# Kernel optimization log

Measured on AMD Instinct MI355X. Metric: run time of the kernel, lower is better.

## Reference

```python
import jax, jax.numpy as jnp
import numpy as np

EPS = 1e-5
GROUPS = 32

def group_norm(x, w, b):
    B, C, H, W = x.shape
    g = GROUPS
    xr = x.reshape(B, g, C // g, H * W)
    mean = xr.mean(axis=(2, 3), keepdims=True)
    var = xr.var(axis=(2, 3), keepdims=True)
    h = ((xr - mean) / jnp.sqrt(var + EPS)).reshape(B, C, H, W)
    return h * w[None, :, None, None] + b[None, :, None, None]

def setup_inputs() -> dict:
    key = jax.random.key(0)
    ks = jax.random.split(key, 7)
    B, C, H, W = 8, 256, 64, 64
    d = C // 8  # 32
    x = jax.random.normal(ks[0], (B, C, H, W), dtype=jnp.float32)
    norm_w = 1.0 + 0.1 * jax.random.normal(ks[1], (C,), dtype=jnp.float32)
    norm_b = 0.1 * jax.random.normal(ks[2], (C,), dtype=jnp.float32)
    s = 1.0 / np.sqrt(C)
    Wq = jax.random.normal(ks[3], (d, C), dtype=jnp.float32) * s
    Wk = jax.random.normal(ks[4], (d, C), dtype=jnp.float32) * s
    Wv = jax.random.normal(ks[5], (C, C), dtype=jnp.float32) * s
    Wproj = jax.random.normal(ks[6], (C, C), dtype=jnp.float32) * s
    gamma = jnp.full((1,), 0.5, dtype=jnp.float32)  # torch init is 0; nonzero so attention path contributes
    return {"x": x, "norm_w": norm_w, "norm_b": norm_b, "Wq": Wq, "Wk": Wk,
            "Wv": Wv, "Wproj": Wproj, "gamma": gamma}

def reference(x, norm_w, norm_b, Wq, Wk, Wv, Wproj, gamma):
    B, C, H, W = x.shape
    N = H * W
    h = group_norm(x, norm_w, norm_b)           # (B,C,H,W)
    hf = h.reshape(B, C, N)                      # flatten spatial
    d = Wq.shape[0]
    q = jnp.einsum('dc,bcn->bnd', Wq, hf)        # (B,N,d)
    k = jnp.einsum('dc,bcn->bdn', Wk, hf)        # (B,d,N)
    v = jnp.einsum('oc,bcn->bno', Wv, hf)        # (B,N,C)
    scale = d ** (-0.5)
    attn = jax.nn.softmax(jnp.einsum('bnd,bdm->bnm', q, k) * scale, axis=-1)  # (B,N,N)
    out = jnp.einsum('bnm,bmo->bno', attn, v)    # (B,N,C)
    out = out.transpose(0, 2, 1).reshape(B, C, H, W)
    proj = jnp.einsum('oc,bchw->bohw', Wproj, out)
    return x + gamma[0] * proj
```

## Files before the change

### kernel.cpp

```cpp
#include <hip/hip_runtime.h>
#include <cstdint>


typedef __bf16 bf16x8 __attribute__((ext_vector_type(8)));
typedef float f32x4 __attribute__((ext_vector_type(4)));
typedef float f32x16 __attribute__((ext_vector_type(16)));
typedef unsigned int u32x4 __attribute__((ext_vector_type(4)));
typedef unsigned short u16x4 __attribute__((ext_vector_type(4)));
typedef unsigned short u16x8 __attribute__((ext_vector_type(8)));

#define DEVI __device__ __forceinline__

DEVI unsigned short f2bf(float f) {
    __bf16 h = (__bf16)f;
    return __builtin_bit_cast(unsigned short, h);
}
DEVI float bf2f(unsigned short u) {
    unsigned int x = ((unsigned int)u) << 16;
    return __builtin_bit_cast(float, x);
}

DEVI f32x4 mfma16(bf16x8 a, bf16x8 b, f32x4 c) {
    return __builtin_amdgcn_mfma_f32_16x16x32_bf16(a, b, c, 0, 0, 0);
}
DEVI f32x16 mfma32(bf16x8 a, bf16x8 b, f32x16 c) {
    return __builtin_amdgcn_mfma_f32_32x32x16_bf16(a, b, c, 0, 0, 0);
}

DEVI void glds16(const unsigned short* g, unsigned short* l) {
    const __attribute__((address_space(1))) unsigned int* gp =
        reinterpret_cast<const __attribute__((address_space(1))) unsigned int*>(
            reinterpret_cast<uintptr_t>(g));
    __attribute__((address_space(3))) unsigned int* lp =
        reinterpret_cast<__attribute__((address_space(3))) unsigned int*>(
            reinterpret_cast<uintptr_t>(l));
    __builtin_amdgcn_global_load_lds(gp, lp, 16, 0, 0);
}

#define QSCALE 0.2550663133f
#define MFIX   12.0f

__global__ __launch_bounds__(256) void k_pack(
        const float* __restrict__ wq, const float* __restrict__ wk,
        const float* __restrict__ wv, const float* __restrict__ wp,
        unsigned short* __restrict__ bqk, unsigned short* __restrict__ bv,
        unsigned short* __restrict__ bp) {
    int i = blockIdx.x * 256 + threadIdx.x;
    if (i < 8192)       bqk[i] = f2bf(wq[i] * QSCALE);
    else if (i < 16384) bqk[i] = f2bf(wk[i - 8192]);
    bv[i] = f2bf(wv[i]);
    bp[i] = f2bf(wp[i]);
}

__global__ __launch_bounds__(1024) void k_gnorm(
        const float* __restrict__ x, const float* __restrict__ gw,
        const float* __restrict__ gb, unsigned short* __restrict__ ht) {
    int bg = blockIdx.x;
    int b = bg >> 5, g = bg & 31;
    const float* xb = x + ((size_t)(b * 256 + g * 8)) * 4096;
    int t = threadIdx.x;
    float s1 = 0.f, s2 = 0.f;
    const f32x4* xv4 = (const f32x4*)xb;
    for (int i = t; i < 8192; i += 1024) {
        f32x4 v = xv4[i];
        #pragma unroll
        for (int j = 0; j < 4; j++) { s1 += v[j]; s2 += v[j] * v[j]; }
    }
    #pragma unroll
    for (int off = 1; off < 64; off <<= 1) {
        s1 += __shfl_xor(s1, off);
        s2 += __shfl_xor(s2, off);
    }
    __shared__ float red[34];
    int wv_ = t >> 6;
    if ((t & 63) == 0) { red[wv_ * 2] = s1; red[wv_ * 2 + 1] = s2; }
    __syncthreads();
    if (t == 0) {
        float a = 0.f, q = 0.f;
        #pragma unroll
        for (int i = 0; i < 16; i++) { a += red[i * 2]; q += red[i * 2 + 1]; }
        float mean = a * (1.f / 32768.f);
        float var = q * (1.f / 32768.f) - mean * mean;
        red[32] = mean; red[33] = rsqrtf(var + 1e-5f);
    }
    __syncthreads();
    float mean = red[32], rstd = red[33];
    float wv8[8], bv8[8];
    #pragma unroll
    for (int c = 0; c < 8; c++) { wv8[c] = gw[g * 8 + c] * rstd; bv8[c] = gb[g * 8 + c] - mean * rstd * gw[g * 8 + c]; }
    int n0 = t * 4;
    f32x4 cv[8];
    #pragma unroll
    for (int c = 0; c < 8; c++) cv[c] = *(const f32x4*)(xb + c * 4096 + n0);
    #pragma unroll
    for (int j = 0; j < 4; j++) {
        u16x8 pk;
        #pragma unroll
        for (int c = 0; c < 8; c++) pk[c] = f2bf(cv[c][j] * wv8[c] + bv8[c]);
        *(u16x8*)(&ht[((size_t)(b * 4096 + n0 + j)) * 256 + g * 8]) = pk;
    }
}

template <int EPI>
__global__ __launch_bounds__(256) void k_gemm(
        const unsigned short* __restrict__ A, const unsigned short* __restrict__ Bw,
        void* __restrict__ outp, const float* __restrict__ xres,
        const float* __restrict__ gamma, int ldout) {
    __shared__ unsigned short lA[128 * 72];
    __shared__ unsigned short lB[64 * 72];
    int t = threadIdx.x;
    int m0 = blockIdx.x * 128, n0 = blockIdx.y * 64;
    int w = t >> 6, lane = t & 63, l15 = lane & 15, quad = lane >> 4;
    f32x4 z4 = {0.f, 0.f, 0.f, 0.f};
    f32x4 acc[2][4];
    #pragma unroll
    for (int i = 0; i < 2; i++)
        #pragma unroll
        for (int j = 0; j < 4; j++) acc[i][j] = z4;

    for (int kb = 0; kb < 4; kb++) {
        #pragma unroll
        for (int i = 0; i < 4; i++) {
            int ch = i * 256 + t;
            int row = ch >> 3, col = (ch & 7) * 8;
            u32x4 v = *(const u32x4*)(A + (size_t)(m0 + row) * 256 + kb * 64 + col);
            *(u32x4*)(&lA[row * 72 + col]) = v;
        }
        #pragma unroll
        for (int i = 0; i < 2; i++) {
            int ch = i * 256 + t;
            int row = ch >> 3, col = (ch & 7) * 8;
            u32x4 v = *(const u32x4*)(Bw + (size_t)(n0 + row) * 256 + kb * 64 + col);
            *(u32x4*)(&lB[row * 72 + col]) = v;
        }
        __syncthreads();
        #pragma unroll
        for (int ks = 0; ks < 2; ks++) {
            bf16x8 af[2], bfr[4];
            #pragma unroll
            for (int fr = 0; fr < 2; fr++)
                af[fr] = *(const bf16x8*)(&lA[(w * 32 + fr * 16 + l15) * 72 + ks * 32 + quad * 8]);
            #pragma unroll
            for (int fn = 0; fn < 4; fn++)
                bfr[fn] = *(const bf16x8*)(&lB[(fn * 16 + l15) * 72 + ks * 32 + quad * 8]);
            #pragma unroll
            for (int fr = 0; fr < 2; fr++)
                #pragma unroll
                for (int fn = 0; fn < 4; fn++)
                    acc[fr][fn] = mfma16(af[fr], bfr[fn], acc[fr][fn]);
        }
        __syncthreads();
    }

    if (EPI == 0) {
        unsigned short* out = (unsigned short*)outp;
        #pragma unroll
        for (int fr = 0; fr < 2; fr++)
            #pragma unroll
            for (int fn = 0; fn < 4; fn++)
                #pragma unroll
                for (int r = 0; r < 4; r++) {
                    int m = m0 + w * 32 + fr * 16 + quad * 4 + r;
                    int n = n0 + fn * 16 + l15;
                    out[(size_t)m * ldout + n] = f2bf(acc[fr][fn][r]);
                }
    } else if (EPI == 1) {
        unsigned short* out = (unsigned short*)outp;
        int b = m0 >> 12, nb = (m0 & 4095) + w * 32;
        int swq = ((quad & 1) << 1) | (quad >> 1);
        #pragma unroll
        for (int fr = 0; fr < 2; fr++)
            #pragma unroll
            for (int fn = 0; fn < 4; fn++) {
                int o = n0 + fn * 16 + l15;
                int n = nb + fr * 16 + swq * 4;
                u16x4 pk;
                #pragma unroll
                for (int r = 0; r < 4; r++) pk[r] = f2bf(acc[fr][fn][r]);
                *(u16x4*)(&out[(((size_t)(b * 256 + o)) << 12) + n]) = pk;
            }
    } else {
        float* out = (float*)outp;
        float gm = gamma[0];
        int b = m0 >> 12, nb = (m0 & 4095) + w * 32;
        #pragma unroll
        for (int fr = 0; fr < 2; fr++)
            #pragma unroll
            for (int fn = 0; fn < 4; fn++) {
                int o = n0 + fn * 16 + l15;
                int n = nb + fr * 16 + quad * 4;
                size_t base = (((size_t)(b * 256 + o)) << 12) + n;
                f32x4 xv = *(const f32x4*)(xres + base);
                f32x4 ov;
                #pragma unroll
                for (int r = 0; r < 4; r++) ov[r] = xv[r] + gm * acc[fr][fn][r];
                *(f32x4*)(out + base) = ov;
            }
    }
}

__global__ __launch_bounds__(256, 2) void k_flash(
        const unsigned short* __restrict__ QK, const unsigned short* __restrict__ Vt,
        unsigned short* __restrict__ Oa) {
    __shared__ __align__(16) char smem[40960];
    unsigned short* lK = (unsigned short*)smem;
    unsigned short* lV = (unsigned short*)(smem + 4096);
    int id = blockIdx.x;
    int b = id & 7, qt = id >> 3;
    int t = threadIdx.x, w = t >> 6, ln = t & 63;
    int l31 = ln & 31, h = ln >> 5;
    int qh = w >> 1, kh = w & 1;
    int q0 = qt * 64;

    const unsigned short* qrow = QK + ((size_t)(b * 4096 + q0 + qh * 32 + l31)) * 64;
    bf16x8 qb0 = *(const bf16x8*)(qrow + h * 8);
    bf16x8 qb1 = *(const bf16x8*)(qrow + 16 + h * 8);

    int cgK = (ln & 3) ^ ((ln >> 2) & 3) ^ ((ln >> 4) & 3);
    const unsigned short* gK = QK + ((size_t)(b * 4096 + w * 16 + (ln >> 2))) * 64 + 32 + cgK * 8;
    unsigned short* sK = lK + w * 512;
    int vc8 = (ln & 7) ^ ((ln >> 3) & 7);
    const unsigned short* gV = Vt + (((size_t)(b * 256 + w * 64 + (ln >> 3))) << 12) + vc8 * 8;
    unsigned short* sV = lV + w * 4096;

    u16x8 onesu = {0x3F80, 0x3F80, 0x3F80, 0x3F80, 0x3F80, 0x3F80, 0x3F80, 0x3F80};
    bf16x8 ones = __builtin_bit_cast(bf16x8, onesu);
    f32x16 z16;
    #pragma unroll
    for (int i = 0; i < 16; i++) z16[i] = 0.f;
    f32x16 minit;
    #pragma unroll
    for (int i = 0; i < 16; i++) minit[i] = -MFIX;
    f32x16 Oacc[8];
    #pragma unroll
    for (int i = 0; i < 8; i++) Oacc[i] = z16;
    f32x16 lacc = z16;

    int gl = (ln & 3) ^ ((ln >> 2) & 3);
    const unsigned short* kf0p = lK + (kh * 32 + l31) * 32 + ((0 + h) ^ gl) * 8;
    const unsigned short* kf1p = lK + (kh * 32 + l31) * 32 + ((2 + h) ^ gl) * 8;

    for (int kt = 0; kt < 64; kt++) {
        glds16(gK + (size_t)kt * 4096, sK);
        #pragma unroll
        for (int j = 0; j < 8; j++)
            glds16(gV + ((size_t)j * 8 << 12) + kt * 64, sV + j * 512);
        __syncthreads();

        bf16x8 kf0 = *(const bf16x8*)kf0p;
        bf16x8 kf1 = *(const bf16x8*)kf1p;
        f32x16 St = mfma32(kf0, qb0, minit);
        St = mfma32(kf1, qb1, St);

        u16x8 p0u, p1u;
        #pragma unroll
        for (int j = 0; j < 8; j++) {
            p0u[j] = f2bf(__builtin_amdgcn_exp2f(St[j]));
            p1u[j] = f2bf(__builtin_amdgcn_exp2f(St[8 + j]));
        }
        bf16x8 pa0 = __builtin_bit_cast(bf16x8, p0u);
        bf16x8 pa1 = __builtin_bit_cast(bf16x8, p1u);

        lacc = mfma32(pa0, ones, lacc);
        lacc = mfma32(pa1, ones, lacc);

        #pragma unroll
        for (int s2 = 0; s2 < 2; s2++) {
            bf16x8 pa = s2 ? pa1 : pa0;
            int slot = ((kh * 4 + s2 * 2 + h) ^ (ln & 7)) * 8;
            #pragma unroll
            for (int nt = 0; nt < 8; nt++) {
                bf16x8 vf = *(const bf16x8*)(lV + (nt * 32 + l31) * 64 + slot);
                Oacc[nt] = mfma32(pa, vf, Oacc[nt]);
            }
        }
        __syncthreads();
    }

    if (kh == 1) {
        #pragma unroll
        for (int nt = 0; nt < 8; nt++)
            #pragma unroll
            for (int rg = 0; rg < 2; rg++) {
                u16x8 pk;
                #pragma unroll
                for (int j = 0; j < 8; j++) pk[j] = f2bf(Oacc[nt][rg * 8 + j]);
                *(u16x8*)(smem + qh * 16384 + nt * 2048 + rg * 1024 + ln * 16) = pk;
            }
        #pragma unroll
        for (int rg = 0; rg < 4; rg++) {
            f32x4 lv;
            #pragma unroll
            for (int j = 0; j < 4; j++) lv[j] = lacc[rg * 4 + j];
            *(f32x4*)(smem + 32768 + qh * 4096 + rg * 1024 + ln * 16) = lv;
        }
    }
    __syncthreads();
    if (kh == 0) {
        float rl[16];
        #pragma unroll
        for (int rg = 0; rg < 4; rg++) {
            f32x4 lv = *(const f32x4*)(smem + 32768 + qh * 4096 + rg * 1024 + ln * 16);
            #pragma unroll
            for (int j = 0; j < 4; j++) rl[rg * 4 + j] = 1.f / (lacc[rg * 4 + j] + lv[j]);
        }
        size_t rb = (size_t)(b * 4096 + q0 + qh * 32);
        #pragma unroll
        for (int nt = 0; nt < 8; nt++)
            #pragma unroll
            for (int rg = 0; rg < 2; rg++) {
                u16x8 pk = *(const u16x8*)(smem + qh * 16384 + nt * 2048 + rg * 1024 + ln * 16);
                #pragma unroll
                for (int j = 0; j < 8; j++) {
                    int r = rg * 8 + j;
                    float val = (Oacc[nt][r] + bf2f(pk[j])) * rl[r];
                    int row = (r & 3) + 8 * (r >> 2) + 4 * h;
                    Oa[(rb + row) * 256 + nt * 32 + l31] = f2bf(val);
                }
            }
    }
}

extern "C" void kernel_launch(void* const* d_in, const int* in_sizes, int n_in,
                              void* d_out, int out_size, void* d_ws, size_t ws_size,
                              hipStream_t stream) {
    const float* x  = (const float*)d_in[0];
    const float* nw = (const float*)d_in[1];
    const float* nb = (const float*)d_in[2];
    const float* wq = (const float*)d_in[3];
    const float* wk = (const float*)d_in[4];
    const float* wv = (const float*)d_in[5];
    const float* wp = (const float*)d_in[6];
    const float* gm = (const float*)d_in[7];

    char* p = (char*)d_ws;
    unsigned short* ht  = (unsigned short*)p; p += (size_t)32768 * 256 * 2;
    unsigned short* qk  = (unsigned short*)p; p += (size_t)32768 * 64 * 2;
    unsigned short* vt  = (unsigned short*)p; p += (size_t)8 * 256 * 4096 * 2;
    unsigned short* oa  = (unsigned short*)p; p += (size_t)32768 * 256 * 2;
    unsigned short* bqk = (unsigned short*)p; p += 64 * 256 * 2;
    unsigned short* bv  = (unsigned short*)p; p += 256 * 256 * 2;
    unsigned short* bp  = (unsigned short*)p; p += 256 * 256 * 2;

    k_pack<<<dim3(256), dim3(256), 0, stream>>>(wq, wk, wv, wp, bqk, bv, bp);
    k_gnorm<<<dim3(256), dim3(1024), 0, stream>>>(x, nw, nb, ht);
    k_gemm<0><<<dim3(256, 1), dim3(256), 0, stream>>>(ht, bqk, (void*)qk, nullptr, nullptr, 64);
    k_gemm<1><<<dim3(256, 4), dim3(256), 0, stream>>>(ht, bv, (void*)vt, nullptr, nullptr, 0);
    k_flash<<<dim3(512), dim3(256), 0, stream>>>(qk, vt, oa);
    k_gemm<2><<<dim3(256, 4), dim3(256), 0, stream>>>(oa, bp, d_out, x, gm, 0);
}
```

Measured before the change: 236.1 us.

## Double-buffer K/V LDS tiles in flash kernel to overlap loads with MFMA

Doubles the flash-attention kernel's shared memory to hold two K/V tile buffers. The loop is unrolled by two so the async global-to-LDS copy of the next tile is issued before computing on the current one. Each step syncs with a raw barrier plus a vmcnt(0) wait instead of two __syncthreads. The goal is to hide global load latency behind the QK/PV MFMA work. The cost is 72KB of LDS per block, which limits occupancy to two blocks per CU.

```diff
diff --git a/kernel.cpp b/kernel.cpp
--- a/kernel.cpp
+++ b/kernel.cpp
@@ -35,6 +35,15 @@
         reinterpret_cast<__attribute__((address_space(3))) unsigned int*>(
             reinterpret_cast<uintptr_t>(l));
     __builtin_amdgcn_global_load_lds(gp, lp, 16, 0, 0);
+}
+
+DEVI void barrier_raw() {
+    asm volatile("" ::: "memory");
+    __builtin_amdgcn_s_barrier();
+    asm volatile("" ::: "memory");
+}
+DEVI void wait_vm0() {
+    __builtin_amdgcn_s_waitcnt(0x3F70);
 }
 
 #define QSCALE 0.2550663133f
@@ -202,9 +211,7 @@
 __global__ __launch_bounds__(256, 2) void k_flash(
         const unsigned short* __restrict__ QK, const unsigned short* __restrict__ Vt,
         unsigned short* __restrict__ Oa) {
-    __shared__ __align__(16) char smem[40960];
-    unsigned short* lK = (unsigned short*)smem;
-    unsigned short* lV = (unsigned short*)(smem + 4096);
+    __shared__ __align__(16) char smem[73728];
     int id = blockIdx.x;
     int b = id & 7, qt = id >> 3;
     int t = threadIdx.x, w = t >> 6, ln = t & 63;
@@ -218,10 +225,17 @@
 
     int cgK = (ln & 3) ^ ((ln >> 2) & 3) ^ ((ln >> 4) & 3);
     const unsigned short* gK = QK + ((size_t)(b * 4096 + w * 16 + (ln >> 2))) * 64 + 32 + cgK * 8;
-    unsigned short* sK = lK + w * 512;
     int vc8 = (ln & 7) ^ ((ln >> 3) & 7);
     const unsigned short* gV = Vt + (((size_t)(b * 256 + w * 64 + (ln >> 3))) << 12) + vc8 * 8;
-    unsigned short* sV = lV + w * 4096;
+
+    unsigned short* lK0 = (unsigned short*)smem;
+    unsigned short* lV0 = (unsigned short*)(smem + 4096);
+    unsigned short* lK1 = (unsigned short*)(smem + 36864);
+    unsigned short* lV1 = (unsigned short*)(smem + 36864 + 4096);
+    unsigned short* sK0 = lK0 + w * 512;
+    unsigned short* sV0 = lV0 + w * 4096;
+    unsigned short* sK1 = lK1 + w * 512;
+    unsigned short* sV1 = lV1 + w * 4096;
 
     u16x8 onesu = {0x3F80, 0x3F80, 0x3F80, 0x3F80, 0x3F80, 0x3F80, 0x3F80, 0x3F80};
     bf16x8 ones = __builtin_bit_cast(bf16x8, onesu);
@@ -236,22 +250,27 @@
     for (int i = 0; i < 8; i++) Oacc[i] = z16;
     f32x16 lacc = z16;
 
-    int gl = (ln & 3) ^ ((ln >> 2) & 3);
-    const unsigned short* kf0p = lK + (kh * 32 + l31) * 32 + ((0 + h) ^ gl) * 8;
-    const unsigned short* kf1p = lK + (kh * 32 + l31) * 32 + ((2 + h) ^ gl) * 8;
-
-    for (int kt = 0; kt < 64; kt++) {
-        glds16(gK + (size_t)kt * 4096, sK);
+    int gl = (l31 & 3) ^ ((l31 >> 2) & 3);
+    const unsigned short* kf0p0 = lK0 + (kh * 32 + l31) * 32 + ((0 + h) ^ gl) * 8;
+    const unsigned short* kf1p0 = lK0 + (kh * 32 + l31) * 32 + ((2 + h) ^ gl) * 8;
+    const unsigned short* kf0p1 = lK1 + (kh * 32 + l31) * 32 + ((0 + h) ^ gl) * 8;
+    const unsigned short* kf1p1 = lK1 + (kh * 32 + l31) * 32 + ((2 + h) ^ gl) * 8;
+    int slotA = ((kh * 4 + 0 * 2 + h) ^ (ln & 7)) * 8;
+    int slotB = ((kh * 4 + 1 * 2 + h) ^ (ln & 7)) * 8;
+
+    auto stage = [&](int kn, unsigned short* sK, unsigned short* sV) {
+        glds16(gK + (size_t)kn * 4096, sK);
         #pragma unroll
         for (int j = 0; j < 8; j++)
-            glds16(gV + ((size_t)j * 8 << 12) + kt * 64, sV + j * 512);
-        __syncthreads();
-
+            glds16(gV + ((size_t)j * 8 << 12) + kn * 64, sV + j * 512);
+    };
+
+    auto compute = [&](const unsigned short* kf0p, const unsigned short* kf1p,
+                       const unsigned short* lV) {
         bf16x8 kf0 = *(const bf16x8*)kf0p;
         bf16x8 kf1 = *(const bf16x8*)kf1p;
         f32x16 St = mfma32(kf0, qb0, minit);
         St = mfma32(kf1, qb1, St);
-
         u16x8 p0u, p1u;
         #pragma unroll
         for (int j = 0; j < 8; j++) {
@@ -260,22 +279,32 @@
         }
         bf16x8 pa0 = __builtin_bit_cast(bf16x8, p0u);
         bf16x8 pa1 = __builtin_bit_cast(bf16x8, p1u);
-
         lacc = mfma32(pa0, ones, lacc);
         lacc = mfma32(pa1, ones, lacc);
-
-        #pragma unroll
-        for (int s2 = 0; s2 < 2; s2++) {
-            bf16x8 pa = s2 ? pa1 : pa0;
-            int slot = ((kh * 4 + s2 * 2 + h) ^ (ln & 7)) * 8;
-            #pragma unroll
-            for (int nt = 0; nt < 8; nt++) {
-                bf16x8 vf = *(const bf16x8*)(lV + (nt * 32 + l31) * 64 + slot);
-                Oacc[nt] = mfma32(pa, vf, Oacc[nt]);
-            }
-        }
-        __syncthreads();
-    }
+        #pragma unroll
+        for (int nt = 0; nt < 8; nt++) {
+            bf16x8 vf = *(const bf16x8*)(lV + (nt * 32 + l31) * 64 + slotA);
+            Oacc[nt] = mfma32(pa0, vf, Oacc[nt]);
+        }
+        #pragma unroll
+        for (int nt = 0; nt < 8; nt++) {
+            bf16x8 vf = *(const bf16x8*)(lV + (nt * 32 + l31) * 64 + slotB);
+            Oacc[nt] = mfma32(pa1, vf, Oacc[nt]);
+        }
+    };
+
+    stage(0, sK0, sV0);
+    for (int kt = 0; kt < 64; kt += 2) {
+        wait_vm0();
+        barrier_raw();
+        stage(kt + 1, sK1, sV1);
+        compute(kf0p0, kf1p0, lV0);
+        wait_vm0();
+        barrier_raw();
+        if (kt + 2 < 64) stage(kt + 2, sK0, sV0);
+        compute(kf0p1, kf1p1, lV1);
+    }
+    __syncthreads();
 
     if (kh == 1) {
         #pragma unroll
```

Result: no change. 234.4 us (-0.8%).
